# Performance work log

Measured on AMD Instinct MI355X. Metric: run time of the kernel, lower is better.

## Reference

```python
import jax, jax.numpy as jnp
import numpy as np

MAX_DUR = 8  # exclusive upper bound used when sampling durations


def setup_inputs() -> dict:
    key = jax.random.key(0)
    k1, k2 = jax.random.split(key)
    B, S, D = 16, 512, 384
    text_emb = jax.random.normal(k1, (B, S, D), dtype=jnp.float32)
    durations = jax.random.randint(k2, (B, S), 0, MAX_DUR, dtype=jnp.int32)
    return {"text_emb": text_emb, "durations": durations}


def reference(text_emb, durations):
    # text_emb: [B, S, D] float32; durations: [B, S] int32
    B, S, D = text_emb.shape
    max_len = S * MAX_DUR  # static padded length (jit-compatible stand-in for pad_sequence)
    # cumulative end offset of each token's expanded span: [B, S]
    cs = jnp.cumsum(durations, axis=1)
    t = jnp.arange(max_len, dtype=cs.dtype)  # output frame positions
    # for each output frame t, source token idx = first j with cs[j] > t
    idx = jax.vmap(lambda c: jnp.searchsorted(c, t, side="right"))(cs)  # [B, max_len]
    total = cs[:, -1:]                      # [B, 1] total expanded length per batch
    valid = t[None, :] < total              # [B, max_len] padding mask
    idx = jnp.clip(idx, 0, S - 1)
    # gather embeddings: [B, max_len, D]
    out = jnp.take_along_axis(text_emb, idx[:, :, None], axis=1)
    return jnp.where(valid[:, :, None], out, jnp.zeros((), dtype=text_emb.dtype))
```

## Files before the change

### kernel.cpp

```cpp
#include <hip/hip_runtime.h>


#define BB 16
#define SS 512
#define DD 384
#define D4 (DD / 4)
#define MAXLEN 4096

__global__ void lr_cumsum_kernel(const int* __restrict__ dur, int* __restrict__ cs) {
    __shared__ int buf[SS];
    const int b = blockIdx.x;
    const int t = threadIdx.x;
    buf[t] = dur[b * SS + t];
    __syncthreads();
    #pragma unroll
    for (int off = 1; off < SS; off <<= 1) {
        int v = (t >= off) ? buf[t - off] : 0;
        __syncthreads();
        buf[t] += v;
        __syncthreads();
    }
    cs[b * SS + t] = buf[t];
}

__global__ void lr_idxmap_kernel(const int* __restrict__ cs, int* __restrict__ idxmap) {
    const int i = blockIdx.x * blockDim.x + threadIdx.x;
    if (i >= BB * MAXLEN) return;
    const int b = i >> 12;
    const int t = i & (MAXLEN - 1);
    const int* c = cs + b * SS;
    const int total = c[SS - 1];
    int lo = 0, hi = SS;
    while (lo < hi) {
        int mid = (lo + hi) >> 1;
        if (c[mid] <= t) lo = mid + 1; else hi = mid;
    }
    int idx = lo;
    if (idx > SS - 1) idx = SS - 1;
    idxmap[i] = (t < total) ? idx : -1;
}

__global__ void lr_gather_kernel(const float4* __restrict__ emb,
                                 const int* __restrict__ idxmap,
                                 float4* __restrict__ out) {
    const int i = blockIdx.x * blockDim.x + threadIdx.x;
    const int d4 = i % D4;
    const int bt = i / D4;
    const int b  = bt >> 12;
    const int idx = idxmap[bt];
    float4 v = make_float4(0.f, 0.f, 0.f, 0.f);
    if (idx >= 0) v = emb[(b * SS + idx) * D4 + d4];
    out[i] = v;
}

extern "C" void kernel_launch(void* const* d_in, const int* in_sizes, int n_in,
                              void* d_out, int out_size, void* d_ws, size_t ws_size,
                              hipStream_t stream) {
    const float* text_emb = (const float*)d_in[0];
    const int*   durations = (const int*)d_in[1];
    float* out = (float*)d_out;

    int* cs     = (int*)d_ws;
    int* idxmap = cs + BB * SS;

    lr_cumsum_kernel<<<BB, SS, 0, stream>>>(durations, cs);

    {
        const int n = BB * MAXLEN;
        lr_idxmap_kernel<<<(n + 255) / 256, 256, 0, stream>>>(cs, idxmap);
    }

    {
        const int n4 = BB * MAXLEN * D4;
        lr_gather_kernel<<<(n4 + 255) / 256, 256, 0, stream>>>(
            (const float4*)text_emb, idxmap, (float4*)out);
    }
}
```

Before: 126.0 us.

## Fuse cumsum, index search and gather into one tiled kernel

Replaces the three-kernel pipeline with one kernel. Each block recomputes the per-batch cumulative sum with a wave-level shuffle scan in LDS, binary-searches source indices for a 128-frame tile, and then gathers embedding rows into the output. This removes two launches and the global round trip of the cumsum and index map. In exchange the scan is redundant across tiles, and the grid is smaller with much more work per thread.

```diff
diff --git a/kernel.cpp b/kernel.cpp
--- a/kernel.cpp
+++ b/kernel.cpp
@@ -6,73 +6,74 @@
 #define DD 384
 #define D4 (DD / 4)
 #define MAXLEN 4096
+#define TILE_T 128
+#define NT (MAXLEN / TILE_T)
+#define NTHREADS 256
 
-__global__ void lr_cumsum_kernel(const int* __restrict__ dur, int* __restrict__ cs) {
-    __shared__ int buf[SS];
-    const int b = blockIdx.x;
-    const int t = threadIdx.x;
-    buf[t] = dur[b * SS + t];
+__global__ __launch_bounds__(NTHREADS)
+void lr_fused_kernel(const float4* __restrict__ emb,
+                     const int* __restrict__ dur,
+                     float4* __restrict__ out) {
+    __shared__ int cs[SS];
+    __shared__ int idx_lds[TILE_T];
+
+    const int blk  = blockIdx.x;
+    const int b    = blk >> 5;
+    const int tile = blk & (NT - 1);
+    const int tid  = threadIdx.x;
+
+    if (tid < 64) {
+        const int* drow = dur + b * SS + tid * 8;
+        int loc[8];
+        int run = 0;
+        #pragma unroll
+        for (int j = 0; j < 8; ++j) { run += drow[j]; loc[j] = run; }
+        int sc = run;
+        #pragma unroll
+        for (int off = 1; off < 64; off <<= 1) {
+            int n = __shfl_up(sc, off, 64);
+            if (tid >= off) sc += n;
+        }
+        const int base = sc - run;
+        #pragma unroll
+        for (int j = 0; j < 8; ++j) cs[tid * 8 + j] = base + loc[j];
+    }
     __syncthreads();
-    #pragma unroll
-    for (int off = 1; off < SS; off <<= 1) {
-        int v = (t >= off) ? buf[t - off] : 0;
-        __syncthreads();
-        buf[t] += v;
-        __syncthreads();
+
+    const int total = cs[SS - 1];
+    const int t0 = tile * TILE_T;
+
+    if (tid < TILE_T) {
+        const int t = t0 + tid;
+        int lo = 0, hi = SS;
+        while (lo < hi) {
+            int mid = (lo + hi) >> 1;
+            if (cs[mid] <= t) lo = mid + 1; else hi = mid;
+        }
+        if (lo > SS - 1) lo = SS - 1;
+        idx_lds[tid] = (t < total) ? lo : -1;
     }
-    cs[b * SS + t] = buf[t];
-}
+    __syncthreads();
 
-__global__ void lr_idxmap_kernel(const int* __restrict__ cs, int* __restrict__ idxmap) {
-    const int i = blockIdx.x * blockDim.x + threadIdx.x;
-    if (i >= BB * MAXLEN) return;
-    const int b = i >> 12;
-    const int t = i & (MAXLEN - 1);
-    const int* c = cs + b * SS;
-    const int total = c[SS - 1];
-    int lo = 0, hi = SS;
-    while (lo < hi) {
-        int mid = (lo + hi) >> 1;
-        if (c[mid] <= t) lo = mid + 1; else hi = mid;
+    const float4* embb = emb + b * SS * D4;
+    float4* outb = out + (size_t)(b * MAXLEN + t0) * D4;
+    const float4 z = make_float4(0.f, 0.f, 0.f, 0.f);
+    #pragma unroll 4
+    for (int j = tid; j < TILE_T * D4; j += NTHREADS) {
+        const int tt  = j / D4;
+        const int d4  = j - tt * D4;
+        const int idx = idx_lds[tt];
+        outb[j] = (idx >= 0) ? embb[idx * D4 + d4] : z;
     }
-    int idx = lo;
-    if (idx > SS - 1) idx = SS - 1;
-    idxmap[i] = (t < total) ? idx : -1;
-}
-
-__global__ void lr_gather_kernel(const float4* __restrict__ emb,
-                                 const int* __restrict__ idxmap,
-                                 float4* __restrict__ out) {
-    const int i = blockIdx.x * blockDim.x + threadIdx.x;
-    const int d4 = i % D4;
-    const int bt = i / D4;
-    const int b  = bt >> 12;
-    const int idx = idxmap[bt];
-    float4 v = make_float4(0.f, 0.f, 0.f, 0.f);
-    if (idx >= 0) v = emb[(b * SS + idx) * D4 + d4];
-    out[i] = v;
 }
 
 extern "C" void kernel_launch(void* const* d_in, const int* in_sizes, int n_in,
                               void* d_out, int out_size, void* d_ws, size_t ws_size,
                               hipStream_t stream) {
-    const float* text_emb = (const float*)d_in[0];
+    const float* text_emb  = (const float*)d_in[0];
     const int*   durations = (const int*)d_in[1];
     float* out = (float*)d_out;
 
-    int* cs     = (int*)d_ws;
-    int* idxmap = cs + BB * SS;
-
-    lr_cumsum_kernel<<<BB, SS, 0, stream>>>(durations, cs);
-
-    {
-        const int n = BB * MAXLEN;
-        lr_idxmap_kernel<<<(n + 255) / 256, 256, 0, stream>>>(cs, idxmap);
-    }
-
-    {
-        const int n4 = BB * MAXLEN * D4;
-        lr_gather_kernel<<<(n4 + 255) / 256, 256, 0, stream>>>(
-            (const float4*)text_emb, idxmap, (float4*)out);
-    }
+    lr_fused_kernel<<<BB * NT, NTHREADS, 0, stream>>>(
+        (const float4*)text_emb, durations, (float4*)out);
 }
```

After: 135.9 us. +7.9%, slower.
